# Optimization experiments

Measured on AMD Instinct MI355X. Metric: run time of the kernel, lower is better.

The kernel has to match this reference:

```python
import jax, jax.numpy as jnp
import numpy as np

DILATIONS = [[1, 2], [4, 8]]
H = 512      # state_hsize
D_IN = 128   # input_size + exogenous_size
OUT = 48     # output_size
T, B = 256, 128


def _lstm(x, W_ih, W_hh, b_ih, b_hh):
    # x: (T2, B2, D). Standard torch nn.LSTM math, gate order i, f, g, o.
    h0 = jnp.zeros((x.shape[1], W_hh.shape[1]), x.dtype)
    b = b_ih + b_hh

    def step(carry, xt):
        h, c = carry
        g = xt @ W_ih.T + h @ W_hh.T + b
        i, f, gg, o = jnp.split(g, 4, axis=-1)
        c = jax.nn.sigmoid(f) * c + jax.nn.sigmoid(i) * jnp.tanh(gg)
        h = jax.nn.sigmoid(o) * jnp.tanh(c)
        return (h, c), h

    _, ys = jax.lax.scan(step, (h0, h0), x)
    return ys


def _drnn_layer(x, rate, W_ih, W_hh, b_ih, b_hh):
    # Dilated RNN layer: interleave time into the batch dim by `rate`,
    # run a plain LSTM, then de-interleave (zalando DRNN scheme).
    T0, B0, D0 = x.shape
    pad = (-T0) % rate
    if pad:
        x = jnp.concatenate([x, jnp.zeros((pad, B0, D0), x.dtype)], 0)
    Tp = T0 + pad
    dil = x.reshape(Tp // rate, rate * B0, D0)   # dil[t, j*B0+b] = x[t*rate+j, b]
    out = _lstm(dil, W_ih, W_hh, b_ih, b_hh)     # (Tp//rate, rate*B0, H)
    out = out.reshape(Tp // rate, rate, B0, -1).reshape(Tp, B0, -1)
    return out[:T0]


def _forward(input_data, Wih, Whh, bih, bhh, mlp_w, mlp_b, adapter_w, adapter_b):
    x = input_data
    k = 0
    for stack_idx, dils in enumerate(DILATIONS):
        residual = x
        h = x
        for d in dils:
            h = _drnn_layer(h, d, Wih[k], Whh[k], bih[k], bhh[k])
            k += 1
        x = h + residual if stack_idx > 0 else h
    x = jnp.tanh(x @ mlp_w.T + mlp_b)
    return x @ adapter_w.T + adapter_b


def setup_inputs() -> dict:
    key = jax.random.key(0)
    ks = jax.random.split(key, 32)

    def gn(k, shape, s=0.05):
        return (jax.random.normal(k, shape) * s).astype(jnp.float32)

    inp = {"input_data": jax.random.normal(ks[0], (T, B, D_IN), jnp.float32)}
    cell_in = [D_IN, H, H, H]  # input dim of each of the 4 LSTM cells
    for i, d in enumerate(cell_in):
        inp[f"W_ih_{i}"] = gn(ks[1 + 4 * i], (4 * H, d))
        inp[f"W_hh_{i}"] = gn(ks[2 + 4 * i], (4 * H, H))
        inp[f"b_ih_{i}"] = gn(ks[3 + 4 * i], (4 * H,))
        inp[f"b_hh_{i}"] = gn(ks[4 + 4 * i], (4 * H,))
    inp["mlp_w"] = gn(ks[20], (H, H))
    inp["mlp_b"] = gn(ks[21], (H,))
    inp["adapter_w"] = gn(ks[22], (OUT, H))
    inp["adapter_b"] = gn(ks[23], (OUT,))
    return inp


def reference(input_data, W_ih_0, W_hh_0, b_ih_0, b_hh_0,
              W_ih_1, W_hh_1, b_ih_1, b_hh_1,
              W_ih_2, W_hh_2, b_ih_2, b_hh_2,
              W_ih_3, W_hh_3, b_ih_3, b_hh_3,
              mlp_w, mlp_b, adapter_w, adapter_b):
    Wih = [W_ih_0, W_ih_1, W_ih_2, W_ih_3]
    Whh = [W_hh_0, W_hh_1, W_hh_2, W_hh_3]
    bih = [b_ih_0, b_ih_1, b_ih_2, b_ih_3]
    bhh = [b_hh_0, b_hh_1, b_hh_2, b_hh_3]
    return _forward(input_data, Wih, Whh, bih, bhh, mlp_w, mlp_b, adapter_w, adapter_b)
```

## Files before the change

kernel.cpp:

```cpp
#include <hip/hip_runtime.h>

#define TPB 512
#define SPIN_BOUND (1u << 20)

typedef _Float16 h8 __attribute__((ext_vector_type(8)));
typedef float f4 __attribute__((ext_vector_type(4)));
typedef unsigned long long u64;

__device__ __forceinline__ float sigf(float x) { return 1.f / (1.f + __expf(-x)); }
__device__ __forceinline__ float tanhfast(float x) { return 2.f / (1.f + __expf(-2.f * x)) - 1.f; }

#define MF(acc, a, b) acc = __builtin_amdgcn_mfma_f32_16x16x32_f16(a, b, acc, 0, 0, 0)

__device__ __forceinline__ void vm0() { asm volatile("s_waitcnt vmcnt(0)" ::: "memory"); }
__device__ __forceinline__ void l1inv() { asm volatile("buffer_inv sc0" ::: "memory"); }
__device__ __forceinline__ void lgkm0() { asm volatile("s_waitcnt lgkmcnt(0)" ::: "memory"); }



__global__ void prep_conv(const float* __restrict__ in, const float* __restrict__ mlpw,
                          const float* __restrict__ adpw,
                          _Float16* __restrict__ seqX, _Float16* __restrict__ mlpW16,
                          _Float16* __restrict__ adpW16)
{
    const int NIN = 256 * 128 * 128;
    const int NM = 512 * 512;
    const int NA = 48 * 512;
    int i = blockIdx.x * blockDim.x + threadIdx.x;
    const int stride = gridDim.x * blockDim.x;
    for (; i < NIN + NM + NA; i += stride) {
        if (i < NIN) seqX[i] = (_Float16)in[i];
        else if (i < NIN + NM) mlpW16[i - NIN] = (_Float16)mlpw[i - NIN];
        else adpW16[i - NIN - NM] = (_Float16)adpw[i - NIN - NM];
    }
}

__global__ void prep_bias(const float* __restrict__ a0, const float* __restrict__ b0,
                          const float* __restrict__ a1, const float* __restrict__ b1,
                          const float* __restrict__ a2, const float* __restrict__ b2,
                          const float* __restrict__ a3, const float* __restrict__ b3,
                          float* __restrict__ biasSum)
{
    int i = blockIdx.x * blockDim.x + threadIdx.x;
    if (i >= 8192) return;
    const int c = i >> 11, j = i & 2047;
    const float* A = (c == 0) ? a0 : (c == 1) ? a1 : (c == 2) ? a2 : a3;
    const float* B = (c == 0) ? b0 : (c == 1) ? b1 : (c == 2) ? b2 : b3;
    biasSum[i] = A[j] + B[j];
}

__global__ void prep_w(const float* __restrict__ wih0, const float* __restrict__ whh0,
                       const float* __restrict__ wih1, const float* __restrict__ whh1,
                       const float* __restrict__ wih2, const float* __restrict__ whh2,
                       const float* __restrict__ wih3, const float* __restrict__ whh3,
                       _Float16* __restrict__ Wprep)
{
    const size_t N0 = (size_t)2048 * 640;
    const size_t N1 = (size_t)2048 * 1024;
    const size_t total = N0 + 3 * N1;
    size_t i = (size_t)blockIdx.x * blockDim.x + threadIdx.x;
    const size_t stride = (size_t)gridDim.x * blockDim.x;
    for (; i < total; i += stride) {
        int cell; size_t off;
        if (i < N0) { cell = 0; off = i; }
        else { cell = 1 + (int)((i - N0) / N1); off = (i - N0) % N1; }
        const int K = cell ? 1024 : 640;
        const int Din = cell ? 512 : 128;
        const int k = (int)(off % K);
        const int rowIdx = (int)(off / K);
        const int p = rowIdx >> 6;
        const int row64 = rowIdx & 63;
        const int q = row64 >> 4;
        const int gRow = q * 512 + p * 16 + (row64 & 15);
        const float* wih = (cell == 0) ? wih0 : (cell == 1) ? wih1 : (cell == 2) ? wih2 : wih3;
        const float* whh = (cell == 0) ? whh0 : (cell == 1) ? whh1 : (cell == 2) ? whh2 : whh3;
        const float v = (k < Din) ? wih[(size_t)gRow * Din + k]
                                  : whh[(size_t)gRow * 512 + (k - Din)];
        Wprep[i] = (_Float16)v;
    }
}


#define SCR_OFF   131072
#define SCRT_OFF  147456
#define MISC_OFF  151552

template<int CELL, int KH, bool XH>
__device__ __forceinline__ void run_cell(
    const _Float16* __restrict__ src, _Float16* __restrict__ dstX,
    const _Float16* __restrict__ wbase, const float* __restrict__ biasSum,
    unsigned* __restrict__ cellFlags, char* smem,
    const int rg, const int p, const int tid, const int lane, const int wave)
{
    constexpr int Din = (CELL == 0) ? 128 : 512;
    constexpr int K = Din + 512;
    constexpr int Bd = 128 << CELL;
    constexpr int PBd = Bd / 2;
    constexpr int Td = 256 >> CELL;
    constexpr int r = Bd >> 3;
    constexpr int nMt = r >> 4;
    constexpr int ldsRow = K * 2;
    constexpr int NKX = Din >> 5;
    constexpr int NXW = NKX / KH;
    constexpr int NHW = 16 / KH;
    constexpr int B1 = (NHW > 8) ? 8 : NHW;
    constexpr int B2 = NHW - B1;
    constexpr int NCOMP = nMt * KH;

    const int colsel = lane & 15;
    const int kq = lane >> 4;
    const int rowBase = rg * r;

    {
        const _Float16* wsl = wbase + (size_t)p * 64 * K;
        constexpr int kcN = K >> 3;
        for (int i = tid; i < 64 * kcN; i += TPB) {
            const int row = i / kcN;
            const int kc = i - row * kcN;
            h8 v = *(const h8*)(wsl + (size_t)row * K + (kc << 3));
            *(h8*)(smem + row * ldsRow + ((kc << 4) ^ ((row & 7) << 4))) = v;
        }
    }
    __syncthreads();

    const int mt = wave / KH;
    const int kh = wave % KH;
    const bool busy = (wave < NCOMP);

    const int xlo = kh * NXW;
    const int hlo = kh * NHW;

    const float bq0 = biasSum[CELL * 2048 + 0 * 512 + p * 16 + colsel];
    const float bq1 = biasSum[CELL * 2048 + 1 * 512 + p * 16 + colsel];
    const float bq2 = biasSum[CELL * 2048 + 2 * 512 + p * 16 + colsel];
    const float bq3 = biasSum[CELL * 2048 + 3 * 512 + p * 16 + colsel];

    const int arow = rowBase + mt * 16 + colsel;

    unsigned* line = cellFlags + (rg * 8 + mt) * 256;
    unsigned* myFlag = line + p * 8;
    float* scr = (float*)(smem + SCR_OFF);
    char* scrT = smem + SCRT_OFF + mt * 512;

    float cr[4] = {0.f, 0.f, 0.f, 0.f};
    bool dead = false;
    h8 xr[(NXW > 0) ? NXW : 1];

    const size_t hOff = (size_t)arow * 16 + (size_t)(kq & 1) * 8 + (size_t)(kq >> 1) * (Bd * 16);
    const int tOff = (arow >= PBd) ? 1 : 0;
    const size_t xBase = (size_t)(arow - tOff * PBd) * 16
                       + (size_t)(kq & 1) * 8 + (size_t)(kq >> 1) * (PBd * 16);

    auto ldB = [&](int kbyte, int rrow) -> h8 {
        return *(const h8*)(smem + rrow * ldsRow + (kbyte ^ ((rrow & 7) << 4)));
    };

    auto wait_line = [&](unsigned tgt) {
        if (dead) return;
        const volatile unsigned* fp = (const volatile unsigned*)(line + (lane & 31) * 8);
        unsigned n = 0;
        for (;;) {
            if (__all((int)(*fp >= tgt))) return;
            l1inv();
            __builtin_amdgcn_s_sleep(1);
            if (++n > SPIN_BOUND) { dead = true; return; }
        }
    };
    auto wait_own = [&](unsigned tgt) {
        if (dead) return;
        const volatile unsigned* f0 = (const volatile unsigned*)myFlag;
        if (*f0 >= tgt) return;
        unsigned n = 0;
        for (;;) {
            l1inv();
            if (*f0 >= tgt) return;
            __builtin_amdgcn_s_sleep(1);
            if (++n > SPIN_BOUND) { dead = true; return; }
        }
    };

    auto x_issue = [&](int t) {
        if constexpr (XH) {
            const char* xp = (const char*)src
                + ((size_t)(2 * t + tOff) * (32 * PBd * 16) + xBase) * 2;
            #pragma unroll
            for (int i = 0; i < NXW; ++i)
                xr[i] = *(const h8*)(xp + (size_t)(xlo + i) * (PBd * 64));
        } else {
            const _Float16* ap = src + (size_t)t * Bd * Din + (size_t)arow * Din + (kq << 3);
            #pragma unroll
            for (int i = 0; i < NXW; ++i)
                xr[i] = *(const h8*)(ap + ((xlo + i) << 5));
        }
    };
    auto x_compute = [&](f4 (&C)[4]) {
        #pragma unroll
        for (int g = 0; g < 4; ++g) C[g] = (f4){0.f, 0.f, 0.f, 0.f};
        #pragma unroll
        for (int i = 0; i < NXW; ++i) {
            const int kbyte = (((xlo + i) << 5) + (kq << 3)) << 1;
            h8 bf0 = ldB(kbyte, colsel);
            h8 bf1 = ldB(kbyte, 16 + colsel);
            h8 bf2 = ldB(kbyte, 32 + colsel);
            h8 bf3 = ldB(kbyte, 48 + colsel);
            MF(C[0], xr[i], bf0); MF(C[1], xr[i], bf1);
            MF(C[2], xr[i], bf2); MF(C[3], xr[i], bf3);
        }
    };
    auto h_mfma = [&](h8 a, int ks, f4 (&C)[4]) {
        const int kbyte = (Din + (ks << 5) + (kq << 3)) << 1;
        h8 bf0 = ldB(kbyte, colsel);
        h8 bf1 = ldB(kbyte, 16 + colsel);
        h8 bf2 = ldB(kbyte, 32 + colsel);
        h8 bf3 = ldB(kbyte, 48 + colsel);
        MF(C[0], a, bf0); MF(C[1], a, bf1); MF(C[2], a, bf2); MF(C[3], a, bf3);
    };
    auto writeScr = [&](f4 (&C)[4]) {
        const int slot = (mt * (KH - 1) + (kh - 1)) * 4;
        #pragma unroll
        for (int g = 0; g < 4; ++g)
            *(f4*)(scr + (size_t)((slot + g) * 64 + lane) * 4) = C[g];
    };
    auto finish = [&](int t, f4 (&C)[4]) {
        if constexpr (KH > 1) {
            #pragma unroll
            for (int s = 0; s < KH - 1; ++s)
                #pragma unroll
                for (int g = 0; g < 4; ++g)
                    C[g] += *(const f4*)(scr + (size_t)(((mt * (KH - 1) + s) * 4 + g) * 64 + lane) * 4);
        }
        _Float16 hf[4];
        #pragma unroll
        for (int j = 0; j < 4; ++j) {
            const float gi = C[0][j] + bq0;
            const float gf = C[1][j] + bq1;
            const float gg = C[2][j] + bq2;
            const float go = C[3][j] + bq3;
            const float cc = sigf(gf) * cr[j] + sigf(gi) * tanhfast(gg);
            cr[j] = cc;
            hf[j] = (_Float16)(sigf(go) * tanhfast(cc));
        }
        #pragma unroll
        for (int j = 0; j < 4; ++j)
            *(_Float16*)(scrT + (kq * 4 + j) * 32 + colsel * 2) = hf[j];
        lgkm0();
        const u64 v = *(const u64*)(scrT + (lane >> 2) * 32 + (lane & 3) * 8);
        const size_t Ebase = ((size_t)t * 32 + p) * (size_t)(Bd * 16)
                           + (size_t)(rowBase + mt * 16) * 16;
        *(u64*)((char*)dstX + Ebase * 2 + (size_t)lane * 8) = v;
        vm0();
        if (lane == 0) *(volatile unsigned*)myFlag = (unsigned)(t + 1);
    };

    f4 acc[4];
    h8 hrA[B1];
    h8 hrB[(B2 > 0) ? B2 : 1];
    if (busy) x_issue(0);

    for (int t = 0; t < Td; ++t) {
        const char* hXp = (const char*)dstX + ((size_t)(t - 1) * (32 * Bd * 16) + hOff) * 2;
        if (busy) {
            x_compute(acc);
            if (t > 0) {
                if constexpr (KH > 1) { if (kh != 0) wait_own((unsigned)t); }
                wait_line((unsigned)t);
                #pragma unroll
                for (int i = 0; i < B1; ++i)
                    hrA[i] = *(const h8*)(hXp + (size_t)(hlo + i) * (Bd * 64));
                if constexpr (B2 > 0) {
                    #pragma unroll
                    for (int i = 0; i < B2; ++i)
                        hrB[i] = *(const h8*)(hXp + (size_t)(hlo + B1 + i) * (Bd * 64));
                }
                #pragma unroll
                for (int i = 0; i < B1; ++i) h_mfma(hrA[i], hlo + i, acc);
                if constexpr (B2 > 0) {
                    #pragma unroll
                    for (int i = 0; i < B2; ++i) h_mfma(hrB[i], hlo + B1 + i, acc);
                }
            }
        }
        if constexpr (KH > 1) {
            if (busy && kh != 0) writeScr(acc);
            __syncthreads();
        }
        if (busy && kh == 0) finish(t, acc);
        if (busy && t + 1 < Td) x_issue(t + 1);
    }
    vm0();
}


__global__ __launch_bounds__(TPB) void drnn_persist(
    const _Float16* __restrict__ seqX,
    _Float16* __restrict__ seq0X,
    _Float16* __restrict__ seq1X,
    _Float16* __restrict__ seq2X,
    _Float16* __restrict__ seq3X,
    const _Float16* __restrict__ Wprep,
    const float* __restrict__ biasSum,
    unsigned* __restrict__ syncc)
{
    extern __shared__ char smem[];
    const int tid = threadIdx.x;
    const int lane = tid & 63;
    const int wave = tid >> 6;

    unsigned* s_misc = (unsigned*)(smem + MISC_OFF);

    if (tid == 0) {
        unsigned xcc;
        asm volatile("s_getreg_b32 %0, hwreg(HW_REG_XCC_ID)" : "=s"(xcc));
        xcc &= 7u;
        unsigned slot = __hip_atomic_fetch_add(syncc + 512u + 64u * xcc, 1u,
                                               __ATOMIC_RELAXED, __HIP_MEMORY_SCOPE_AGENT);
        s_misc[0] = (xcc << 5) | (slot & 31u);
    }
    __syncthreads();
    const unsigned rgp = s_misc[0];
    __syncthreads();
    const int rg = rgp >> 5;
    const int p = rgp & 31;

    unsigned* cellCnt = syncc;
    unsigned* flags = syncc + 4096;

    auto cell_barrier = [&](int cellIdx, unsigned TdPrev, int nMtPrev, unsigned* flagsPrev) {
        __syncthreads();
        if (p == 0 && tid < 32 * nMtPrev) {
            const volatile unsigned* fp =
                (const volatile unsigned*)(flagsPrev + (rg * 8 + (tid >> 5)) * 256 + (tid & 31) * 8);
            unsigned n = 0;
            for (;;) {
                l1inv();
                if (*fp >= TdPrev) break;
                __builtin_amdgcn_s_sleep(1);
                if (++n > SPIN_BOUND) break;
            }
        }
        __syncthreads();
        if (tid == 0) {
            if (p == 0)
                __hip_atomic_fetch_add(cellCnt, 1u, __ATOMIC_RELEASE, __HIP_MEMORY_SCOPE_AGENT);
            unsigned n = 0;
            while (__hip_atomic_load(cellCnt, __ATOMIC_RELAXED, __HIP_MEMORY_SCOPE_AGENT)
                   < (unsigned)(8 * cellIdx)) {
                __builtin_amdgcn_s_sleep(1);
                if (++n > SPIN_BOUND) break;
            }
            (void)__hip_atomic_load(cellCnt, __ATOMIC_ACQUIRE, __HIP_MEMORY_SCOPE_AGENT);
        }
        __syncthreads();
        l1inv();
    };

    run_cell<0, 2, false>(seqX,  seq0X, Wprep,                        biasSum, flags + 0 * 16384, smem, rg, p, tid, lane, wave);
    cell_barrier(1, 256u, 1, flags + 0 * 16384);
    run_cell<1, 2, true >(seq0X, seq1X, Wprep + (size_t)2048 * 640,   biasSum, flags + 1 * 16384, smem, rg, p, tid, lane, wave);
    cell_barrier(2, 128u, 2, flags + 1 * 16384);
    run_cell<2, 2, true >(seq1X, seq2X, Wprep + (size_t)2048 * 1664,  biasSum, flags + 2 * 16384, smem, rg, p, tid, lane, wave);
    cell_barrier(3, 64u, 4, flags + 2 * 16384);
    run_cell<3, 1, true >(seq2X, seq3X, Wprep + (size_t)2048 * 2688,  biasSum, flags + 3 * 16384, smem, rg, p, tid, lane, wave);
}


__global__ __launch_bounds__(256) void head_kernel(
    const _Float16* __restrict__ seq1X,
    const _Float16* __restrict__ seq3X,
    const _Float16* __restrict__ mlpW16,
    const float* __restrict__ mlp_b,
    const _Float16* __restrict__ adpW16,
    const float* __restrict__ adp_b,
    float* __restrict__ out)
{
    extern __shared__ char smem[];
    const int tid = threadIdx.x;
    const int lane = tid & 63, wave = tid >> 6;
    const int colsel = lane & 15, kq = lane >> 4;
    const size_t row0 = (size_t)blockIdx.x * 64 + wave * 16;

    h8 aR[16];
    {
        const size_t R = row0 + colsel;
        const size_t off1 = ((R >> 8) * 32 + (size_t)(kq >> 1)) * 4096
                          + (R & 255) * 16 + (size_t)(kq & 1) * 8;
        const size_t off3 = ((R >> 10) * 32 + (size_t)(kq >> 1)) * 16384
                          + (R & 1023) * 16 + (size_t)(kq & 1) * 8;
        #pragma unroll
        for (int ks = 0; ks < 16; ++ks) {
            h8 a1 = *(const h8*)(seq1X + off1 + (size_t)ks * 8192);
            h8 a3 = *(const h8*)(seq3X + off3 + (size_t)ks * 32768);
            aR[ks] = a1 + a3;
        }
    }
    for (int nt = 0; nt < 32; ++nt) {
        f4 acc = {0.f, 0.f, 0.f, 0.f};
        const int brow = nt * 16 + colsel;
        #pragma unroll
        for (int ks = 0; ks < 16; ++ks) {
            const int kb = ks * 32 + kq * 8;
            h8 b = *(const h8*)(mlpW16 + (size_t)brow * 512 + kb);
            acc = __builtin_amdgcn_mfma_f32_16x16x32_f16(aR[ks], b, acc, 0, 0, 0);
        }
        const int n = nt * 16 + colsel;
        const float bn = mlp_b[n];
        const int lrow0 = wave * 16 + kq * 4;
        #pragma unroll
        for (int j = 0; j < 4; ++j) {
            const float y = tanhfast(acc[j] + bn);
            const int row = lrow0 + j;
            *(_Float16*)(smem + row * 1024 + ((n * 2) ^ ((row & 7) << 4))) = (_Float16)y;
        }
    }
    __syncthreads();
    f4 acc0 = {0.f,0.f,0.f,0.f}, acc1 = {0.f,0.f,0.f,0.f}, acc2 = {0.f,0.f,0.f,0.f};
    const int arow = wave * 16 + colsel;
    #pragma unroll
    for (int ks = 0; ks < 16; ++ks) {
        const int kb = ks * 32 + kq * 8;
        h8 a = *(const h8*)(smem + arow * 1024 + ((kb * 2) ^ ((arow & 7) << 4)));
        h8 b0 = *(const h8*)(adpW16 + (size_t)(colsel) * 512 + kb);
        h8 b1 = *(const h8*)(adpW16 + (size_t)(16 + colsel) * 512 + kb);
        h8 b2 = *(const h8*)(adpW16 + (size_t)(32 + colsel) * 512 + kb);
        acc0 = __builtin_amdgcn_mfma_f32_16x16x32_f16(a, b0, acc0, 0, 0, 0);
        acc1 = __builtin_amdgcn_mfma_f32_16x16x32_f16(a, b1, acc1, 0, 0, 0);
        acc2 = __builtin_amdgcn_mfma_f32_16x16x32_f16(a, b2, acc2, 0, 0, 0);
    }
    const size_t orow0 = row0 + kq * 4;
    #pragma unroll
    for (int j = 0; j < 4; ++j) {
        out[(orow0 + j) * 48 + colsel]      = acc0[j] + adp_b[colsel];
        out[(orow0 + j) * 48 + 16 + colsel] = acc1[j] + adp_b[16 + colsel];
        out[(orow0 + j) * 48 + 32 + colsel] = acc2[j] + adp_b[32 + colsel];
    }
}


extern "C" void kernel_launch(void* const* d_in, const int* in_sizes, int n_in,
                              void* d_out, int out_size, void* d_ws, size_t ws_size,
                              hipStream_t stream)
{
    (void)in_sizes; (void)n_in; (void)out_size; (void)ws_size;
    const float* input = (const float*)d_in[0];
    const float* Wih[4]; const float* Whh[4]; const float* Bih[4]; const float* Bhh[4];
    for (int i = 0; i < 4; ++i) {
        Wih[i] = (const float*)d_in[1 + 4 * i];
        Whh[i] = (const float*)d_in[2 + 4 * i];
        Bih[i] = (const float*)d_in[3 + 4 * i];
        Bhh[i] = (const float*)d_in[4 + 4 * i];
    }
    const float* mlpw = (const float*)d_in[17];
    const float* mlpb = (const float*)d_in[18];
    const float* adpw = (const float*)d_in[19];
    const float* adpb = (const float*)d_in[20];
    float* out = (float*)d_out;

    char* ws = (char*)d_ws;
    size_t off = 0;
    auto alloc = [&](size_t bytes) -> char* {
        char* ptr = ws + off;
        off += (bytes + 255) & ~(size_t)255;
        return ptr;
    };
    const size_t SEQB = (size_t)32768 * 512 * 2;
    const size_t SYNC_BYTES = (size_t)(4096 + 4 * 16384) * 4;
    unsigned* syncc   = (unsigned*)alloc(SYNC_BYTES);
    _Float16* seqX    = (_Float16*)alloc((size_t)32768 * 128 * 2);
    _Float16* seq0X   = (_Float16*)alloc(SEQB);
    _Float16* seq1X   = (_Float16*)alloc(SEQB);
    _Float16* seq2X   = (_Float16*)alloc(SEQB);
    _Float16* seq3X   = (_Float16*)alloc(SEQB);
    _Float16* Wprep   = (_Float16*)alloc((size_t)2048 * 3712 * 2);
    float*    biasSum = (float*)alloc(8192 * 4);
    _Float16* mlpW16  = (_Float16*)alloc((size_t)262144 * 2);
    _Float16* adpW16  = (_Float16*)alloc((size_t)24576 * 2);

    hipMemsetAsync(syncc, 0, SYNC_BYTES, stream);
    prep_conv<<<2048, 256, 0, stream>>>(input, mlpw, adpw, seqX, mlpW16, adpW16);
    prep_bias<<<32, 256, 0, stream>>>(Bih[0], Bhh[0], Bih[1], Bhh[1],
                                      Bih[2], Bhh[2], Bih[3], Bhh[3], biasSum);
    prep_w<<<4096, 256, 0, stream>>>(Wih[0], Whh[0], Wih[1], Whh[1],
                                     Wih[2], Whh[2], Wih[3], Whh[3], Wprep);

    const int ldsBytes = MISC_OFF + 128;
    hipFuncSetAttribute((const void*)drnn_persist,
                        hipFuncAttributeMaxDynamicSharedMemorySize, ldsBytes);
    hipFuncSetAttribute((const void*)head_kernel,
                        hipFuncAttributeMaxDynamicSharedMemorySize, 65536);

    drnn_persist<<<256, TPB, ldsBytes, stream>>>(seqX, seq0X, seq1X, seq2X, seq3X,
                                                 Wprep, biasSum, syncc);
    head_kernel<<<512, 256, 65536, stream>>>(seq1X, seq3X, mlpW16, mlpb, adpW16, adpb, out);
}
```

Before: 2.012 ms.

## Pad sync flags to 128B, split recurrent K unevenly, overlap h loads with x compute

Widens each per-block progress flag stride from 32 bytes to 128 bytes so spinning waves poll separate cache lines, and grows the flag buffer to match. Moves the input-projection MFMAs after the wait on the previous hidden state so they overlap the global loads of h. Splits the recurrent K work unevenly (6 chunks to the finishing wave, 10 to the helper) so the wave doing the gate math has less MFMA work on the critical path. The trade-off is a larger flag buffer and the x projection now waiting for the sync, which could lengthen the per-step path if the loads return quickly.

```diff
diff --git a/kernel.cpp b/kernel.cpp
--- a/kernel.cpp
+++ b/kernel.cpp
@@ -85,6 +85,15 @@
 #define SCRT_OFF  147456
 #define MISC_OFF  151552
 
+#define H_LOAD(arr, HLO, HN_)                                          \
+    _Pragma("unroll")                                                  \
+    for (int i_ = 0; i_ < (HN_); ++i_)                                 \
+        arr[i_] = *(const h8*)(hXp + (size_t)((HLO) + i_) * (Bd * 64));
+
+#define H_MFMA_ALL(arr, HLO, HN_)                                      \
+    _Pragma("unroll")                                                  \
+    for (int i_ = 0; i_ < (HN_); ++i_) h_mfma(arr[i_], (HLO) + i_, acc);
+
 template<int CELL, int KH, bool XH>
 __device__ __forceinline__ void run_cell(
     const _Float16* __restrict__ src, _Float16* __restrict__ dstX,
@@ -102,10 +111,8 @@
     constexpr int ldsRow = K * 2;
     constexpr int NKX = Din >> 5;
     constexpr int NXW = NKX / KH;
-    constexpr int NHW = 16 / KH;
-    constexpr int B1 = (NHW > 8) ? 8 : NHW;
-    constexpr int B2 = NHW - B1;
     constexpr int NCOMP = nMt * KH;
+    constexpr int HSPL = 6;
 
     const int colsel = lane & 15;
     const int kq = lane >> 4;
@@ -128,7 +135,6 @@
     const bool busy = (wave < NCOMP);
 
     const int xlo = kh * NXW;
-    const int hlo = kh * NHW;
 
     const float bq0 = biasSum[CELL * 2048 + 0 * 512 + p * 16 + colsel];
     const float bq1 = biasSum[CELL * 2048 + 1 * 512 + p * 16 + colsel];
@@ -137,8 +143,8 @@
 
     const int arow = rowBase + mt * 16 + colsel;
 
-    unsigned* line = cellFlags + (rg * 8 + mt) * 256;
-    unsigned* myFlag = line + p * 8;
+    unsigned* line = cellFlags + (rg * 8 + mt) * 1024;
+    unsigned* myFlag = line + p * 32;
     float* scr = (float*)(smem + SCR_OFF);
     char* scrT = smem + SCRT_OFF + mt * 512;
 
@@ -157,7 +163,7 @@
 
     auto wait_line = [&](unsigned tgt) {
         if (dead) return;
-        const volatile unsigned* fp = (const volatile unsigned*)(line + (lane & 31) * 8);
+        const volatile unsigned* fp = (const volatile unsigned*)(line + (lane & 31) * 32);
         unsigned n = 0;
         for (;;) {
             if (__all((int)(*fp >= tgt))) return;
@@ -253,30 +259,36 @@
     };
 
     f4 acc[4];
-    h8 hrA[B1];
-    h8 hrB[(B2 > 0) ? B2 : 1];
+    h8 hrA[8];
+    h8 hrB[8];
     if (busy) x_issue(0);
 
     for (int t = 0; t < Td; ++t) {
         const char* hXp = (const char*)dstX + ((size_t)(t - 1) * (32 * Bd * 16) + hOff) * 2;
         if (busy) {
-            x_compute(acc);
-            if (t > 0) {
-                if constexpr (KH > 1) { if (kh != 0) wait_own((unsigned)t); }
+            if (t == 0) {
+                x_compute(acc);
+            } else if constexpr (KH == 1) {
                 wait_line((unsigned)t);
-                #pragma unroll
-                for (int i = 0; i < B1; ++i)
-                    hrA[i] = *(const h8*)(hXp + (size_t)(hlo + i) * (Bd * 64));
-                if constexpr (B2 > 0) {
-                    #pragma unroll
-                    for (int i = 0; i < B2; ++i)
-                        hrB[i] = *(const h8*)(hXp + (size_t)(hlo + B1 + i) * (Bd * 64));
-                }
-                #pragma unroll
-                for (int i = 0; i < B1; ++i) h_mfma(hrA[i], hlo + i, acc);
-                if constexpr (B2 > 0) {
-                    #pragma unroll
-                    for (int i = 0; i < B2; ++i) h_mfma(hrB[i], hlo + B1 + i, acc);
+                H_LOAD(hrA, 0, 8)
+                x_compute(acc);
+                H_LOAD(hrB, 8, 8)
+                H_MFMA_ALL(hrA, 0, 8)
+                H_MFMA_ALL(hrB, 8, 8)
+            } else {
+                if (kh == 0) {
+                    wait_line((unsigned)t);
+                    H_LOAD(hrA, 0, HSPL)
+                    x_compute(acc);
+                    H_MFMA_ALL(hrA, 0, HSPL)
+                } else {
+                    wait_own((unsigned)t);
+                    wait_line((unsigned)t);
+                    H_LOAD(hrA, HSPL, 8)
+                    x_compute(acc);
+                    H_LOAD(hrB, HSPL + 8, 16 - HSPL - 8)
+                    H_MFMA_ALL(hrA, HSPL, 8)
+                    H_MFMA_ALL(hrB, HSPL + 8, 16 - HSPL - 8)
                 }
             }
         }
@@ -329,7 +341,7 @@
         __syncthreads();
         if (p == 0 && tid < 32 * nMtPrev) {
             const volatile unsigned* fp =
-                (const volatile unsigned*)(flagsPrev + (rg * 8 + (tid >> 5)) * 256 + (tid & 31) * 8);
+                (const volatile unsigned*)(flagsPrev + (rg * 8 + (tid >> 5)) * 1024 + (tid & 31) * 32);
             unsigned n = 0;
             for (;;) {
                 l1inv();
@@ -354,13 +366,13 @@
         l1inv();
     };
 
-    run_cell<0, 2, false>(seqX,  seq0X, Wprep,                        biasSum, flags + 0 * 16384, smem, rg, p, tid, lane, wave);
-    cell_barrier(1, 256u, 1, flags + 0 * 16384);
-    run_cell<1, 2, true >(seq0X, seq1X, Wprep + (size_t)2048 * 640,   biasSum, flags + 1 * 16384, smem, rg, p, tid, lane, wave);
-    cell_barrier(2, 128u, 2, flags + 1 * 16384);
-    run_cell<2, 2, true >(seq1X, seq2X, Wprep + (size_t)2048 * 1664,  biasSum, flags + 2 * 16384, smem, rg, p, tid, lane, wave);
-    cell_barrier(3, 64u, 4, flags + 2 * 16384);
-    run_cell<3, 1, true >(seq2X, seq3X, Wprep + (size_t)2048 * 2688,  biasSum, flags + 3 * 16384, smem, rg, p, tid, lane, wave);
+    run_cell<0, 2, false>(seqX,  seq0X, Wprep,                        biasSum, flags + 0 * 65536, smem, rg, p, tid, lane, wave);
+    cell_barrier(1, 256u, 1, flags + 0 * 65536);
+    run_cell<1, 2, true >(seq0X, seq1X, Wprep + (size_t)2048 * 640,   biasSum, flags + 1 * 65536, smem, rg, p, tid, lane, wave);
+    cell_barrier(2, 128u, 2, flags + 1 * 65536);
+    run_cell<2, 2, true >(seq1X, seq2X, Wprep + (size_t)2048 * 1664,  biasSum, flags + 2 * 65536, smem, rg, p, tid, lane, wave);
+    cell_barrier(3, 64u, 4, flags + 2 * 65536);
+    run_cell<3, 1, true >(seq2X, seq3X, Wprep + (size_t)2048 * 2688,  biasSum, flags + 3 * 65536, smem, rg, p, tid, lane, wave);
 }
 
 
@@ -463,7 +475,7 @@
         return ptr;
     };
     const size_t SEQB = (size_t)32768 * 512 * 2;
-    const size_t SYNC_BYTES = (size_t)(4096 + 4 * 16384) * 4;
+    const size_t SYNC_BYTES = (size_t)(4096 + 4 * 65536) * 4;
     unsigned* syncc   = (unsigned*)alloc(SYNC_BYTES);
     _Float16* seqX    = (_Float16*)alloc((size_t)32768 * 128 * 2);
     _Float16* seq0X   = (_Float16*)alloc(SEQB);
```

Result: slower. 2.170 ms (+7.9%).
